# Kernel optimization log

Hardware: AMD Instinct MI355X
Metric: run time of the kernel (lower is better)

The kernel has to match this reference:

```python
import jax, jax.numpy as jnp
import numpy as np

UP = 2
KSIZE = 3
RES = 64
LRELU_SLOPE = 0.2
ACT_GAIN = float(np.sqrt(2.0))  # def_gain of 'lrelu' in bias_act


def _setup_filter():
    # upfirdn2d.setup_filter([1,3,3,1]): normalize, make separable 2D filter
    f = jnp.array([1.0, 3.0, 3.0, 1.0], dtype=jnp.float32)
    f = f / jnp.sum(f)
    return jnp.outer(f, f)  # [4,4]


def _upfirdn2d_up2(x, f2):
    # Zero-insertion upsample by 2 + pad + FIR filter, gain = up**2.
    # Torch path: zero-insert to 2H, pad (3,2), conv 4-tap -> 2H+2.
    # lhs_dilation gives 2H-1; absorbing the trailing inserted zero into the
    # right pad ((3,3) instead of (3,2)) is exactly equivalent.
    B, C, H, W = x.shape
    k = (f2 * (UP * UP)).astype(x.dtype)[None, None]  # [1,1,4,4] (symmetric, flip-invariant)
    k = jnp.tile(k, (C, 1, 1, 1))                     # depthwise [C,1,4,4]
    return jax.lax.conv_general_dilated(
        x, k, window_strides=(1, 1), padding=((3, 3), (3, 3)),
        lhs_dilation=(UP, UP),
        dimension_numbers=('NCHW', 'OIHW', 'NCHW'),
        feature_group_count=C)


def setup_inputs() -> dict:
    key = jax.random.key(0)
    ks = jax.random.split(key, 6)
    B, Cin, Cout, Wd = 16, 512, 512, 512
    Hin = RES // UP
    return {
        "x": jax.random.normal(ks[0], (B, Cin, Hin, Hin), jnp.float32),
        "w": jax.random.normal(ks[1], (B, Wd), jnp.float32),
        "affine_weight": jax.random.normal(ks[2], (Cin, Wd), jnp.float32),
        "affine_bias": jnp.ones((Cin,), jnp.float32),  # bias_init=1
        "weight": jax.random.normal(ks[3], (Cout, Cin, KSIZE, KSIZE), jnp.float32),
        "bias": jnp.zeros((Cout,), jnp.float32),
        "noise_const": jax.random.normal(ks[4], (RES, RES), jnp.float32),
        "noise_strength": jax.random.uniform(ks[5], (), jnp.float32),
    }


def reference(x, w, affine_weight, affine_bias, weight, bias, noise_const, noise_strength):
    B, Cin, Hin, Win = x.shape
    Cout = weight.shape[0]
    # affine: FullyConnectedLayer, weight_gain = 1/sqrt(w_dim), bias_init=1
    styles = w @ affine_weight.T * (1.0 / np.sqrt(w.shape[1])) + affine_bias  # [B,Cin]
    # modulate + demodulate (fused_modconv=True): per-sample weights
    wmod = weight[None] * styles[:, None, :, None, None]                     # [B,Cout,Cin,kh,kw]
    dcoef = jax.lax.rsqrt(jnp.sum(jnp.square(wmod), axis=(2, 3, 4)) + 1e-8)  # [B,Cout]
    wmod = wmod * dcoef[:, :, None, None, None]
    # up=2 -> flip_weight=False -> true convolution: flip spatial taps
    wmod = wmod[..., ::-1, ::-1]
    # conv2d_resample: upfirdn2d upsample first (pad = k//2 + (fw+up-1)//2 = 3), then VALID conv
    xu = _upfirdn2d_up2(x, _setup_filter())                                  # [B,Cin,66,66]
    xr = xu.reshape(1, B * Cin, xu.shape[2], xu.shape[3])
    wr = wmod.reshape(B * Cout, Cin, KSIZE, KSIZE)
    y = jax.lax.conv_general_dilated(
        xr, wr, window_strides=(1, 1), padding='VALID',
        dimension_numbers=('NCHW', 'OIHW', 'NCHW'),
        feature_group_count=B)
    y = y.reshape(B, Cout, RES, RES)
    # noise_mode='const': noise = noise_const * noise_strength
    y = y + noise_const * noise_strength
    # fused bias + lrelu + def_gain (gain=1, conv_clamp=None)
    y = jax.nn.leaky_relu(y + bias[None, :, None, None], LRELU_SLOPE) * ACT_GAIN
    return y
```

## Files before the change

kernel.cpp:

```cpp
#include <hip/hip_runtime.h>
#include <hip/hip_bf16.h>
#include <math.h>

#define CIN   512
#define COUT  512
#define NB    16
#define WD    512
#define HIN   32
#define HUP   66
#define RES   64
#define LRELU 0.2f
#define ACT_GAIN 1.4142135623730951f

typedef __attribute__((ext_vector_type(8))) short short8;
typedef __attribute__((ext_vector_type(4))) float float4v;
typedef __attribute__((ext_vector_type(16))) float float16v;

__global__ void styles2_kernel(const float* __restrict__ w,
                               const float* __restrict__ aw,
                               const float* __restrict__ ab,
                               float* __restrict__ styles) {
    int b = blockIdx.x;
    int cig = blockIdx.y;
    int lane = threadIdx.x & 63, wv = threadIdx.x >> 6;
    __shared__ float wsh[WD];
    for (int e = threadIdx.x; e < WD; e += 256) wsh[e] = w[b * WD + e];
    __syncthreads();
    for (int r = 0; r < 16; ++r) {
        int ci = cig * 64 + wv * 16 + r;
        const float* arow = aw + (size_t)ci * WD;
        float acc = 0.f;
        for (int k = lane; k < WD; k += 64) acc += arow[k] * wsh[k];
        for (int off = 32; off; off >>= 1) acc += __shfl_down(acc, off, 64);
        if (lane == 0)
            styles[b * CIN + ci] = acc * 0.04419417382415922f + ab[ci];
    }
}

__global__ void prep_weights(const float* __restrict__ weight,
                             float* __restrict__ wsq,
                             __hip_bfloat16* __restrict__ wb) {
    int idx = blockIdx.x * 256 + threadIdx.x;
    int co = idx & (COUT - 1);
    int ci = idx >> 9;
    const float* wp = weight + ((size_t)co * CIN + ci) * 9;
    int cc = ci >> 5, chi = (ci >> 3) & 3, clo = ci & 7;
    float s = 0.f;
#pragma unroll
    for (int t = 0; t < 9; ++t) {
        float v = wp[t];
        s += v * v;
        int tf = 8 - t;
        wb[((((size_t)cc * 9 + tf) * 4 + chi) * COUT + co) * 8 + clo] = __float2bfloat16(v);
    }
    wsq[(size_t)co * CIN + ci] = s;
}

__global__ void dcoef2_kernel(const float* __restrict__ styles,
                              const float* __restrict__ wsq,
                              float* __restrict__ dcoef) {
    int b = blockIdx.x;
    int cog = blockIdx.y;
    int lane = threadIdx.x & 63, wv = threadIdx.x >> 6;
    __shared__ float s2[CIN];
    for (int e = threadIdx.x; e < CIN; e += 256) {
        float s = styles[b * CIN + e];
        s2[e] = s * s;
    }
    __syncthreads();
    for (int r = 0; r < 16; ++r) {
        int co = cog * 64 + wv * 16 + r;
        const float* qrow = wsq + (size_t)co * CIN;
        float acc = 0.f;
        for (int k = lane; k < CIN; k += 64) acc += qrow[k] * s2[k];
        for (int off = 32; off; off >>= 1) acc += __shfl_down(acc, off, 64);
        if (lane == 0) dcoef[b * COUT + co] = rsqrtf(acc + 1e-8f);
    }
}

__global__ void upmod2_kernel(const float* __restrict__ x,
                              const float* __restrict__ styles,
                              __hip_bfloat16* __restrict__ xs2) {
    __shared__ float xt[128 * 68];
    __shared__ float ssh[128];
    __shared__ __align__(16) char ob[66 * 272];
    const int oh = blockIdx.x;
    const int ci0 = blockIdx.y * 128;
    const int b = blockIdx.z;
    int m0, m1; float a0, a1;
    if (oh & 1) { m0 = (oh - 3) >> 1; a0 = 0.125f; m1 = (oh - 1) >> 1; a1 = 0.375f; }
    else        { m0 = (oh >> 1) - 1; a0 = 0.375f; m1 = (oh >> 1);     a1 = 0.125f; }
    if (threadIdx.x < 128) ssh[threadIdx.x] = styles[b * CIN + ci0 + threadIdx.x] * 4.0f;
    for (int e = threadIdx.x; e < 2048; e += 256) {
        int ci = e >> 4, sel = (e >> 3) & 1, iw4 = e & 7;
        int m = sel ? m1 : m0;
        float4v v = (float4v)0.f;
        if (m >= 0 && m < HIN)
            v = *(const float4v*)(x + ((size_t)(b * CIN + ci0 + ci) * HIN + m) * HIN + iw4 * 4);
        *(float4v*)(&xt[ci * 68 + sel * 32 + iw4 * 4]) = v;
    }
    __syncthreads();
    for (int e = threadIdx.x; e < 1056; e += 256) {
        int cig = e / 66;
        int ow = e - cig * 66;
        int n0i, n1i; float b0, b1;
        if (ow & 1) { n0i = (ow - 3) >> 1; b0 = 0.125f; n1i = (ow - 1) >> 1; b1 = 0.375f; }
        else        { n0i = (ow >> 1) - 1; b0 = 0.375f; n1i = (ow >> 1);     b1 = 0.125f; }
        bool c0 = (n0i >= 0) & (n0i < HIN);
        bool c1 = (n1i >= 0) & (n1i < HIN);
        short8 sv;
#pragma unroll
        for (int u = 0; u < 8; ++u) {
            int ci = cig * 8 + u;
            const float* base = &xt[ci * 68];
            float r0 = (c0 ? base[n0i] : 0.f) * b0 + (c1 ? base[n1i] : 0.f) * b1;
            float r1 = (c0 ? base[32 + n0i] : 0.f) * b0 + (c1 ? base[32 + n1i] : 0.f) * b1;
            float val = (a0 * r0 + a1 * r1) * ssh[ci];
            __hip_bfloat16 h = __float2bfloat16(val);
            sv[u] = *reinterpret_cast<const short*>(&h);
        }
        *reinterpret_cast<short8*>(ob + ow * 272 + cig * 16) = sv;
    }
    __syncthreads();
    for (int e = threadIdx.x; e < 1056; e += 256) {
        int ow = e >> 4, t16 = e & 15;
        short8 v = *reinterpret_cast<const short8*>(ob + ow * 272 + t16 * 16);
        *reinterpret_cast<short8*>(
            xs2 + (((size_t)b * HUP + oh) * HUP + ow) * CIN + ci0 + t16 * 8) = v;
    }
}

#define ABUF 43008
#define BBUF 36864
#define BUFSZ (ABUF + BBUF)
#define LDS_TOT (2 * BUFSZ)

__global__ __launch_bounds__(512, 1) void conv_mfma(
        const __hip_bfloat16* __restrict__ xs2,
        const __hip_bfloat16* __restrict__ wb,
        const float* __restrict__ dcoef,
        const float* __restrict__ bias,
        const float* __restrict__ noise,
        const float* __restrict__ nstr,
        float* __restrict__ out)
{
    extern __shared__ __align__(16) char smem[];
    const int tid = threadIdx.x;
    const int lane = tid & 63;
    const int wid = tid >> 6;
    const int li32 = lane & 31;
    const int hi = lane >> 5;
    const int mb = blockIdx.x;
    const int n0 = blockIdx.y * 64;
    const int b  = blockIdx.z;
    const int y0 = mb * 8;

    int a_goff[6];
#pragma unroll
    for (int k = 0; k < 6; ++k) {
        int n = wid + k * 8;
        int s = n * 64 + lane;
        if (s > 2639) s = 2639;
        int r = s / 264;
        int rem = s - r * 264;
        int chi = rem / 66;
        int col = rem - chi * 66;
        a_goff[k] = ((b * HUP + y0 + r) * HUP + col) * CIN + chi * 8;
    }
    int b_goff[5];
#pragma unroll
    for (int k = 0; k < 5; ++k) {
        int sl = wid + k * 8;
        b_goff[k] = (sl * COUT + n0 + lane) * 8;
    }

    float16v acc[2][2];
#pragma unroll
    for (int i = 0; i < 2; ++i)
#pragma unroll
        for (int j = 0; j < 2; ++j) acc[i][j] = (float16v)0.f;

    const char* xg = (const char*)xs2;
    const char* wg = (const char*)wb;

#define STAGE(CC, BUFB) do {                                                  \
        _Pragma("unroll")                                                     \
        for (int k = 0; k < 5; ++k) {                                         \
            int sl = wid + k * 8;                                             \
            if (sl < 36) {                                                    \
                long ge = (long)(b_goff[k] + (CC) * 147456);                  \
                __builtin_amdgcn_global_load_lds(                             \
                    (const __attribute__((address_space(1))) char*)(wg + ge * 2), \
                    (__attribute__((address_space(3))) char*)(smem + (BUFB) + ABUF + sl * 1024), \
                    16, 0, 0);                                                \
            }                                                                 \
        }                                                                     \
        _Pragma("unroll")                                                     \
        for (int k = 0; k < 6; ++k) {                                         \
            int n = wid + k * 8;                                              \
            if (n < 42) {                                                     \
                long ge = (long)(a_goff[k] + (CC) * 32);                      \
                __builtin_amdgcn_global_load_lds(                             \
                    (const __attribute__((address_space(1))) char*)(xg + ge * 2), \
                    (__attribute__((address_space(3))) char*)(smem + (BUFB) + n * 1024), \
                    16, 0, 0);                                                \
            }                                                                 \
        }                                                                     \
    } while (0)

#define LOADF(BUFB, S, SLOT) do {                                             \
        const int t_ = (S) >> 1, ks_ = (S) & 1;                               \
        const int kh_ = t_ / 3, kw_ = t_ - kh_ * 3;                           \
        _Pragma("unroll")                                                     \
        for (int nf = 0; nf < 2; ++nf)                                        \
            fB[SLOT][nf] = *(const short8*)(smem + (BUFB) + ABUF +            \
                    (((t_ * 4 + ks_ * 2 + hi) * 64) + nf * 32 + li32) * 16);  \
        _Pragma("unroll")                                                     \
        for (int mf = 0; mf < 2; ++mf)                                        \
            fA[SLOT][mf] = *(const short8*)(smem + (BUFB) +                   \
                    ((((wid + kh_) * 4 + ks_ * 2 + hi) * 66) +                \
                     (mf * 32 + li32 + kw_)) * 16);                           \
    } while (0)

#define COMPUTE(BUFB) do {                                                    \
        short8 fA[2][2], fB[2][2];                                            \
        LOADF(BUFB, 0, 0);                                                    \
        __builtin_amdgcn_sched_group_barrier(0x100, 4, 0);    \
        __builtin_amdgcn_s_setprio(1);                                        \
        _Pragma("unroll")                                                     \
        for (int s = 0; s < 18; ++s) {                                        \
            const int cur = s & 1, nxt = cur ^ 1;                             \
            if (s < 17) LOADF(BUFB, s + 1, nxt);                              \
            _Pragma("unroll")                                                 \
            for (int mf = 0; mf < 2; ++mf)                                    \
                _Pragma("unroll")                                             \
                for (int nf = 0; nf < 2; ++nf)                                \
                    acc[mf][nf] = __builtin_amdgcn_mfma_f32_32x32x16_bf16(    \
                        fA[cur][mf], fB[cur][nf], acc[mf][nf], 0, 0, 0);      \
            if (s < 17)                                                       \
                __builtin_amdgcn_sched_group_barrier(0x100, 4, 0);  \
            __builtin_amdgcn_sched_group_barrier(0x008, 4, 0);      \
        }                                                                     \
        __builtin_amdgcn_s_setprio(0);                                        \
    } while (0)

#define SYNC() do {                                                           \
        asm volatile("s_waitcnt vmcnt(0)" ::: "memory");                      \
        __builtin_amdgcn_s_barrier();                                         \
    } while (0)

    STAGE(0, 0);
    SYNC();

#pragma unroll 1
    for (int cc = 0; cc < 16; cc += 2) {
        STAGE(cc + 1, BUFSZ);
        COMPUTE(0);
        SYNC();
        if (cc + 2 < 16) STAGE(cc + 2, 0);
        COMPUTE(BUFSZ);
        SYNC();
    }

#undef STAGE
#undef LOADF
#undef COMPUTE
#undef SYNC

    const float ns = nstr[0];
    const int row = y0 + wid;
#pragma unroll
    for (int nf = 0; nf < 2; ++nf) {
        int cout = n0 + nf * 32 + li32;
        float dc = dcoef[b * COUT + cout];
        float bs = bias[cout];
        float* op = out + ((size_t)(b * COUT + cout) * RES + row) * RES;
#pragma unroll
        for (int mf = 0; mf < 2; ++mf) {
#pragma unroll
            for (int r2 = 0; r2 < 4; ++r2) {
                int x0 = mf * 32 + hi * 4 + r2 * 8;
                float4v nz = *(const float4v*)(noise + row * RES + x0);
                float4v r;
                r.x = acc[mf][nf][r2 * 4 + 0] * dc + nz.x * ns + bs;
                r.y = acc[mf][nf][r2 * 4 + 1] * dc + nz.y * ns + bs;
                r.z = acc[mf][nf][r2 * 4 + 2] * dc + nz.z * ns + bs;
                r.w = acc[mf][nf][r2 * 4 + 3] * dc + nz.w * ns + bs;
                r.x = (r.x > 0.f ? r.x : LRELU * r.x) * ACT_GAIN;
                r.y = (r.y > 0.f ? r.y : LRELU * r.y) * ACT_GAIN;
                r.z = (r.z > 0.f ? r.z : LRELU * r.z) * ACT_GAIN;
                r.w = (r.w > 0.f ? r.w : LRELU * r.w) * ACT_GAIN;
                *(float4v*)(op + x0) = r;
            }
        }
    }
}

extern "C" void kernel_launch(void* const* d_in, const int* in_sizes, int n_in,
                              void* d_out, int out_size, void* d_ws, size_t ws_size,
                              hipStream_t stream) {
    (void)in_sizes; (void)n_in; (void)out_size; (void)ws_size;
    const float* x     = (const float*)d_in[0];
    const float* w     = (const float*)d_in[1];
    const float* aw    = (const float*)d_in[2];
    const float* ab    = (const float*)d_in[3];
    const float* wt    = (const float*)d_in[4];
    const float* bias  = (const float*)d_in[5];
    const float* noise = (const float*)d_in[6];
    const float* nstr  = (const float*)d_in[7];
    float* out = (float*)d_out;

    static bool init = false;
    if (!init) {
        hipFuncSetAttribute(reinterpret_cast<const void*>(conv_mfma),
                            hipFuncAttributeMaxDynamicSharedMemorySize, LDS_TOT);
        init = true;
    }

    char* ws = (char*)d_ws;
    float* styles = (float*)ws;
    float* dcoef  = (float*)(ws + 32768);
    float* wsq    = (float*)(ws + 65536);
    __hip_bfloat16* wb  = (__hip_bfloat16*)(ws + 65536 + 1048576);
    __hip_bfloat16* xs2 = (__hip_bfloat16*)(ws + 65536 + 1048576 + 4718592);

    styles2_kernel<<<dim3(NB, 8), dim3(256), 0, stream>>>(w, aw, ab, styles);
    prep_weights<<<dim3(1024), dim3(256), 0, stream>>>(wt, wsq, wb);
    dcoef2_kernel<<<dim3(NB, 8), dim3(256), 0, stream>>>(styles, wsq, dcoef);
    upmod2_kernel<<<dim3(HUP, 4, NB), dim3(256), 0, stream>>>(x, styles, xs2);
    conv_mfma<<<dim3(8, 8, NB), dim3(512), LDS_TOT, stream>>>(
        xs2, wb, dcoef, bias, noise, nstr, out);
}
```

Measured before the change: 509.4 us.

## Fold FIR upsample into polyphase conv weights, convolving on low-res input

The upsample FIR filter is folded into the 3x3 modulated weights, giving four polyphase 3x3 kernels that are applied directly to the padded 34x34 low-res input. This removes the explicit 66x66 upsampled intermediate and its global traffic, and the upsample kernel becomes a simple style-scale and pad pass. The conv grid splits by phase and each block writes strided output columns. The cost is a fourfold larger prepared weight buffer and scalar, non-vectorized output stores.

```diff
diff --git a/kernel.cpp b/kernel.cpp
--- a/kernel.cpp
+++ b/kernel.cpp
@@ -7,7 +7,6 @@
 #define NB    16
 #define WD    512
 #define HIN   32
-#define HUP   66
 #define RES   64
 #define LRELU 0.2f
 #define ACT_GAIN 1.4142135623730951f
@@ -39,21 +38,54 @@
 
 __global__ void prep_weights(const float* __restrict__ weight,
                              float* __restrict__ wsq,
-                             __hip_bfloat16* __restrict__ wb) {
+                             __hip_bfloat16* __restrict__ gb) {
     int idx = blockIdx.x * 256 + threadIdx.x;
     int co = idx & (COUT - 1);
     int ci = idx >> 9;
     const float* wp = weight + ((size_t)co * CIN + ci) * 9;
+    float wv[3][3];
+    float s = 0.f;
+#pragma unroll
+    for (int ay = 0; ay < 3; ++ay)
+#pragma unroll
+        for (int ax = 0; ax < 3; ++ax) {
+            float v = wp[ay * 3 + ax];
+            wv[ay][ax] = v;
+            s += v * v;
+        }
+    wsq[(size_t)co * CIN + ci] = s;
+
+    const float cr[2][3][3] = {
+        {{0.f, 0.25f, 0.75f}, {0.75f, 0.75f, 0.25f}, {0.25f, 0.f, 0.f}},
+        {{0.f, 0.f, 0.25f},  {0.25f, 0.75f, 0.75f}, {0.75f, 0.25f, 0.f}}};
+
     int cc = ci >> 5, chi = (ci >> 3) & 3, clo = ci & 7;
-    float s = 0.f;
-#pragma unroll
-    for (int t = 0; t < 9; ++t) {
-        float v = wp[t];
-        s += v * v;
-        int tf = 8 - t;
-        wb[((((size_t)cc * 9 + tf) * 4 + chi) * COUT + co) * 8 + clo] = __float2bfloat16(v);
-    }
-    wsq[(size_t)co * CIN + ci] = s;
+#pragma unroll
+    for (int phy = 0; phy < 2; ++phy) {
+        float tmp[3][3];
+#pragma unroll
+        for (int dy = 0; dy < 3; ++dy)
+#pragma unroll
+            for (int ax = 0; ax < 3; ++ax)
+                tmp[dy][ax] = cr[phy][dy][0] * wv[0][ax]
+                            + cr[phy][dy][1] * wv[1][ax]
+                            + cr[phy][dy][2] * wv[2][ax];
+#pragma unroll
+        for (int phx = 0; phx < 2; ++phx) {
+            int ph = phy * 2 + phx;
+#pragma unroll
+            for (int dy = 0; dy < 3; ++dy)
+#pragma unroll
+                for (int dx = 0; dx < 3; ++dx) {
+                    float g = tmp[dy][0] * cr[phx][dx][0]
+                            + tmp[dy][1] * cr[phx][dx][1]
+                            + tmp[dy][2] * cr[phx][dx][2];
+                    int t = dy * 3 + dx;
+                    gb[((((size_t)cc * 4 + ph) * 9 + t) * 4 + chi) * (COUT * 8)
+                       + (size_t)co * 8 + clo] = __float2bfloat16(g);
+                }
+        }
+    }
 }
 
 __global__ void dcoef2_kernel(const float* __restrict__ styles,
@@ -78,66 +110,49 @@
     }
 }
 
-__global__ void upmod2_kernel(const float* __restrict__ x,
-                              const float* __restrict__ styles,
-                              __hip_bfloat16* __restrict__ xs2) {
-    __shared__ float xt[128 * 68];
+__global__ void xmod_kernel(const float* __restrict__ x,
+                            const float* __restrict__ styles,
+                            __hip_bfloat16* __restrict__ xb) {
+    __shared__ float xt[128 * 36];
     __shared__ float ssh[128];
-    __shared__ __align__(16) char ob[66 * 272];
-    const int oh = blockIdx.x;
+    const int r = blockIdx.x;
     const int ci0 = blockIdx.y * 128;
     const int b = blockIdx.z;
-    int m0, m1; float a0, a1;
-    if (oh & 1) { m0 = (oh - 3) >> 1; a0 = 0.125f; m1 = (oh - 1) >> 1; a1 = 0.375f; }
-    else        { m0 = (oh >> 1) - 1; a0 = 0.375f; m1 = (oh >> 1);     a1 = 0.125f; }
-    if (threadIdx.x < 128) ssh[threadIdx.x] = styles[b * CIN + ci0 + threadIdx.x] * 4.0f;
-    for (int e = threadIdx.x; e < 2048; e += 256) {
-        int ci = e >> 4, sel = (e >> 3) & 1, iw4 = e & 7;
-        int m = sel ? m1 : m0;
-        float4v v = (float4v)0.f;
-        if (m >= 0 && m < HIN)
-            v = *(const float4v*)(x + ((size_t)(b * CIN + ci0 + ci) * HIN + m) * HIN + iw4 * 4);
-        *(float4v*)(&xt[ci * 68 + sel * 32 + iw4 * 4]) = v;
+    if (threadIdx.x < 128) ssh[threadIdx.x] = styles[b * CIN + ci0 + threadIdx.x];
+    const bool inr = (r >= 1) && (r <= 32);
+    if (inr) {
+        for (int e = threadIdx.x; e < 1024; e += 256) {
+            int ci = e >> 3, iw4 = e & 7;
+            float4v v = *(const float4v*)(
+                x + ((size_t)(b * CIN + ci0 + ci) * HIN + (r - 1)) * HIN + iw4 * 4);
+            *(float4v*)(&xt[ci * 36 + iw4 * 4]) = v;
+        }
     }
     __syncthreads();
-    for (int e = threadIdx.x; e < 1056; e += 256) {
-        int cig = e / 66;
-        int ow = e - cig * 66;
-        int n0i, n1i; float b0, b1;
-        if (ow & 1) { n0i = (ow - 3) >> 1; b0 = 0.125f; n1i = (ow - 1) >> 1; b1 = 0.375f; }
-        else        { n0i = (ow >> 1) - 1; b0 = 0.375f; n1i = (ow >> 1);     b1 = 0.125f; }
-        bool c0 = (n0i >= 0) & (n0i < HIN);
-        bool c1 = (n1i >= 0) & (n1i < HIN);
+    for (int e = threadIdx.x; e < 544; e += 256) {
+        int c = e >> 4, t16 = e & 15;
         short8 sv;
 #pragma unroll
         for (int u = 0; u < 8; ++u) {
-            int ci = cig * 8 + u;
-            const float* base = &xt[ci * 68];
-            float r0 = (c0 ? base[n0i] : 0.f) * b0 + (c1 ? base[n1i] : 0.f) * b1;
-            float r1 = (c0 ? base[32 + n0i] : 0.f) * b0 + (c1 ? base[32 + n1i] : 0.f) * b1;
-            float val = (a0 * r0 + a1 * r1) * ssh[ci];
+            int ci = t16 * 8 + u;
+            float val = 0.f;
+            if (inr && c >= 1 && c <= 32) val = xt[ci * 36 + (c - 1)] * ssh[ci];
             __hip_bfloat16 h = __float2bfloat16(val);
             sv[u] = *reinterpret_cast<const short*>(&h);
         }
-        *reinterpret_cast<short8*>(ob + ow * 272 + cig * 16) = sv;
-    }
-    __syncthreads();
-    for (int e = threadIdx.x; e < 1056; e += 256) {
-        int ow = e >> 4, t16 = e & 15;
-        short8 v = *reinterpret_cast<const short8*>(ob + ow * 272 + t16 * 16);
         *reinterpret_cast<short8*>(
-            xs2 + (((size_t)b * HUP + oh) * HUP + ow) * CIN + ci0 + t16 * 8) = v;
-    }
-}
-
-#define ABUF 43008
+            xb + (((size_t)b * 34 + r) * 34 + c) * CIN + ci0 + t16 * 8) = sv;
+    }
+}
+
+#define ABUF 39936
 #define BBUF 36864
 #define BUFSZ (ABUF + BBUF)
 #define LDS_TOT (2 * BUFSZ)
 
 __global__ __launch_bounds__(512, 1) void conv_mfma(
-        const __hip_bfloat16* __restrict__ xs2,
-        const __hip_bfloat16* __restrict__ wb,
+        const __hip_bfloat16* __restrict__ xb,
+        const __hip_bfloat16* __restrict__ gb,
         const float* __restrict__ dcoef,
         const float* __restrict__ bias,
         const float* __restrict__ noise,
@@ -152,20 +167,23 @@
     const int hi = lane >> 5;
     const int mb = blockIdx.x;
     const int n0 = blockIdx.y * 64;
-    const int b  = blockIdx.z;
-    const int y0 = mb * 8;
-
-    int a_goff[6];
-#pragma unroll
-    for (int k = 0; k < 6; ++k) {
+    const int bz = blockIdx.z;
+    const int b  = bz >> 2;
+    const int ph = bz & 3;
+    const int phy = ph >> 1, phx = ph & 1;
+    const int y0 = mb * 16;
+
+    int a_goff[5];
+#pragma unroll
+    for (int k = 0; k < 5; ++k) {
         int n = wid + k * 8;
         int s = n * 64 + lane;
-        if (s > 2639) s = 2639;
-        int r = s / 264;
-        int rem = s - r * 264;
-        int chi = rem / 66;
-        int col = rem - chi * 66;
-        a_goff[k] = ((b * HUP + y0 + r) * HUP + col) * CIN + chi * 8;
+        if (s > 2447) s = 2447;
+        int cr = s / 136;
+        int rem = s - cr * 136;
+        int chi = rem / 34;
+        int col = rem - chi * 34;
+        a_goff[k] = (((b * 34 + y0 + cr) * 34 + col)) * CIN + chi * 8;
     }
     int b_goff[5];
 #pragma unroll
@@ -180,15 +198,15 @@
 #pragma unroll
         for (int j = 0; j < 2; ++j) acc[i][j] = (float16v)0.f;
 
-    const char* xg = (const char*)xs2;
-    const char* wg = (const char*)wb;
+    const char* xg = (const char*)xb;
+    const char* wg = (const char*)gb;
 
 #define STAGE(CC, BUFB) do {                                                  \
         _Pragma("unroll")                                                     \
         for (int k = 0; k < 5; ++k) {                                         \
             int sl = wid + k * 8;                                             \
             if (sl < 36) {                                                    \
-                long ge = (long)(b_goff[k] + (CC) * 147456);                  \
+                long ge = (long)b_goff[k] + (long)((CC) * 4 + ph) * 147456;   \
                 __builtin_amdgcn_global_load_lds(                             \
                     (const __attribute__((address_space(1))) char*)(wg + ge * 2), \
                     (__attribute__((address_space(3))) char*)(smem + (BUFB) + ABUF + sl * 1024), \
@@ -196,9 +214,9 @@
             }                                                                 \
         }                                                                     \
         _Pragma("unroll")                                                     \
-        for (int k = 0; k < 6; ++k) {                                         \
+        for (int k = 0; k < 5; ++k) {                                         \
             int n = wid + k * 8;                                              \
-            if (n < 42) {                                                     \
+            if (n < 39) {                                                     \
                 long ge = (long)(a_goff[k] + (CC) * 32);                      \
                 __builtin_amdgcn_global_load_lds(                             \
                     (const __attribute__((address_space(1))) char*)(xg + ge * 2), \
@@ -210,7 +228,7 @@
 
 #define LOADF(BUFB, S, SLOT) do {                                             \
         const int t_ = (S) >> 1, ks_ = (S) & 1;                               \
-        const int kh_ = t_ / 3, kw_ = t_ - kh_ * 3;                           \
+        const int dy1 = t_ / 3, dx1 = t_ - dy1 * 3;                           \
         _Pragma("unroll")                                                     \
         for (int nf = 0; nf < 2; ++nf)                                        \
             fB[SLOT][nf] = *(const short8*)(smem + (BUFB) + ABUF +            \
@@ -218,8 +236,8 @@
         _Pragma("unroll")                                                     \
         for (int mf = 0; mf < 2; ++mf)                                        \
             fA[SLOT][mf] = *(const short8*)(smem + (BUFB) +                   \
-                    ((((wid + kh_) * 4 + ks_ * 2 + hi) * 66) +                \
-                     (mf * 32 + li32 + kw_)) * 16);                           \
+                    ((((wid * 2 + mf + dy1) * 4 + ks_ * 2 + hi) * 34) +       \
+                     (li32 + dx1)) * 16);                                     \
     } while (0)
 
 #define COMPUTE(BUFB) do {                                                    \
@@ -268,29 +286,27 @@
 #undef SYNC
 
     const float ns = nstr[0];
-    const int row = y0 + wid;
 #pragma unroll
     for (int nf = 0; nf < 2; ++nf) {
         int cout = n0 + nf * 32 + li32;
         float dc = dcoef[b * COUT + cout];
         float bs = bias[cout];
-        float* op = out + ((size_t)(b * COUT + cout) * RES + row) * RES;
 #pragma unroll
         for (int mf = 0; mf < 2; ++mf) {
+            int ic = y0 + wid * 2 + mf;
+            int fr = 2 * ic + phy;
+            float* op = out + ((size_t)(b * COUT + cout) * RES + fr) * RES;
+            const float* npz = noise + fr * RES;
 #pragma unroll
             for (int r2 = 0; r2 < 4; ++r2) {
-                int x0 = mf * 32 + hi * 4 + r2 * 8;
-                float4v nz = *(const float4v*)(noise + row * RES + x0);
-                float4v r;
-                r.x = acc[mf][nf][r2 * 4 + 0] * dc + nz.x * ns + bs;
-                r.y = acc[mf][nf][r2 * 4 + 1] * dc + nz.y * ns + bs;
-                r.z = acc[mf][nf][r2 * 4 + 2] * dc + nz.z * ns + bs;
-                r.w = acc[mf][nf][r2 * 4 + 3] * dc + nz.w * ns + bs;
-                r.x = (r.x > 0.f ? r.x : LRELU * r.x) * ACT_GAIN;
-                r.y = (r.y > 0.f ? r.y : LRELU * r.y) * ACT_GAIN;
-                r.z = (r.z > 0.f ? r.z : LRELU * r.z) * ACT_GAIN;
-                r.w = (r.w > 0.f ? r.w : LRELU * r.w) * ACT_GAIN;
-                *(float4v*)(op + x0) = r;
+#pragma unroll
+                for (int u = 0; u < 4; ++u) {
+                    int j = 8 * r2 + 4 * hi + u;
+                    int fc = 2 * j + phx;
+                    float v = acc[mf][nf][r2 * 4 + u] * dc + npz[fc] * ns + bs;
+                    v = (v > 0.f ? v : LRELU * v) * ACT_GAIN;
+                    op[fc] = v;
+                }
             }
         }
     }
@@ -321,13 +337,13 @@
     float* styles = (float*)ws;
     float* dcoef  = (float*)(ws + 32768);
     float* wsq    = (float*)(ws + 65536);
-    __hip_bfloat16* wb  = (__hip_bfloat16*)(ws + 65536 + 1048576);
-    __hip_bfloat16* xs2 = (__hip_bfloat16*)(ws + 65536 + 1048576 + 4718592);
+    __hip_bfloat16* gb = (__hip_bfloat16*)(ws + 65536 + 1048576);
+    __hip_bfloat16* xb = (__hip_bfloat16*)(ws + 65536 + 1048576 + 18874368);
 
     styles2_kernel<<<dim3(NB, 8), dim3(256), 0, stream>>>(w, aw, ab, styles);
-    prep_weights<<<dim3(1024), dim3(256), 0, stream>>>(wt, wsq, wb);
+    prep_weights<<<dim3(1024), dim3(256), 0, stream>>>(wt, wsq, gb);
     dcoef2_kernel<<<dim3(NB, 8), dim3(256), 0, stream>>>(styles, wsq, dcoef);
-    upmod2_kernel<<<dim3(HUP, 4, NB), dim3(256), 0, stream>>>(x, styles, xs2);
-    conv_mfma<<<dim3(8, 8, NB), dim3(512), LDS_TOT, stream>>>(
-        xs2, wb, dcoef, bias, noise, nstr, out);
-}
+    xmod_kernel<<<dim3(34, 4, NB), dim3(256), 0, stream>>>(x, styles, xb);
+    conv_mfma<<<dim3(2, 8, NB * 4), dim3(512), LDS_TOT, stream>>>(
+        xb, gb, dcoef, bias, noise, nstr, out);
+}
```

Measured after the change: 557.4 us. +9.4%, slower.
